# Optimization experiments

Hardware: AMD Instinct MI355X
Metric: run time of the kernel (lower is better)

Reference implementation:

```python
import jax, jax.numpy as jnp
import numpy as np

D_MODEL = 1024
NUM_HEADS = 16
D_K = D_MODEL // NUM_HEADS
D_FF = 4096
B, S = 4, 2048
EPS = 1e-5


def _linear_params(key, d_in, d_out):
    # torch nn.Linear default init: U(-1/sqrt(d_in), 1/sqrt(d_in))
    k1, k2 = jax.random.split(key)
    bound = 1.0 / np.sqrt(d_in)
    W = jax.random.uniform(k1, (d_in, d_out), jnp.float32, -bound, bound)
    b = jax.random.uniform(k2, (d_out,), jnp.float32, -bound, bound)
    return W, b


def setup_inputs() -> dict:
    key = jax.random.key(0)
    ks = jax.random.split(key, 8)
    x = jax.random.normal(ks[0], (B, S, D_MODEL), jnp.float32)
    Wq, bq = _linear_params(ks[1], D_MODEL, D_MODEL)
    Wk, bk = _linear_params(ks[2], D_MODEL, D_MODEL)
    Wv, bv = _linear_params(ks[3], D_MODEL, D_MODEL)
    Wo, bo = _linear_params(ks[4], D_MODEL, D_MODEL)
    W1, b1 = _linear_params(ks[5], D_MODEL, D_FF)
    W2, b2 = _linear_params(ks[6], D_FF, D_MODEL)
    ln1_g = jnp.ones((D_MODEL,), jnp.float32)
    ln1_b = jnp.zeros((D_MODEL,), jnp.float32)
    ln2_g = jnp.ones((D_MODEL,), jnp.float32)
    ln2_b = jnp.zeros((D_MODEL,), jnp.float32)
    return dict(x=x, Wq=Wq, bq=bq, Wk=Wk, bk=bk, Wv=Wv, bv=bv, Wo=Wo, bo=bo,
                W1=W1, b1=b1, W2=W2, b2=b2,
                ln1_g=ln1_g, ln1_b=ln1_b, ln2_g=ln2_g, ln2_b=ln2_b)


def _layernorm(x, g, b):
    mu = jnp.mean(x, axis=-1, keepdims=True)
    var = jnp.mean(jnp.square(x - mu), axis=-1, keepdims=True)
    return (x - mu) * jax.lax.rsqrt(var + EPS) * g + b


def _attention(h, Wq, bq, Wk, bk, Wv, bv, Wo, bo):
    b, s, _ = h.shape
    def split_heads(t):  # (b,s,d) -> (b,H,s,dk)
        return t.reshape(b, s, NUM_HEADS, D_K).transpose(0, 2, 1, 3)
    Q = split_heads(h @ Wq + bq)
    K = split_heads(h @ Wk + bk)
    V = split_heads(h @ Wv + bv)
    scores = jnp.einsum('bhqd,bhkd->bhqk', Q, K) / np.sqrt(D_K)
    causal = jnp.tril(jnp.ones((s, s), dtype=bool))  # True = keep
    scores = jnp.where(causal, scores, -jnp.inf)
    attn = jax.nn.softmax(scores, axis=-1)
    out = jnp.einsum('bhqk,bhkd->bhqd', attn, V)
    out = out.transpose(0, 2, 1, 3).reshape(b, s, D_MODEL)
    return out @ Wo + bo


def reference(x, Wq, bq, Wk, bk, Wv, bv, Wo, bo, W1, b1, W2, b2,
              ln1_g, ln1_b, ln2_g, ln2_b):
    # pre-norm residual block
    x = x + _attention(_layernorm(x, ln1_g, ln1_b), Wq, bq, Wk, bk, Wv, bv, Wo, bo)
    h = _layernorm(x, ln2_g, ln2_b)
    x = x + (jax.nn.relu(h @ W1 + b1) @ W2 + b2)
    return x
```

## Files before the change

kernel.cpp:

```cpp
#include <hip/hip_runtime.h>
#include <hip/hip_bf16.h>

typedef __bf16 bf16;
typedef __attribute__((ext_vector_type(8))) __bf16 bf16x8;
typedef __attribute__((ext_vector_type(4))) float f32x4;

#define D_MODEL 1024
#define NHEADS  16
#define DK      64
#define DFF     4096
#define BATCH   4
#define SEQ     2048
#define NTOK    (BATCH*SEQ)
#define QSCALE  0.18033688011112042f

__device__ __forceinline__ void gload16(const bf16* g, bf16* l) {
    __builtin_amdgcn_global_load_lds((const __attribute__((address_space(1))) void*)g,
                                     (__attribute__((address_space(3))) void*)l, 16, 0, 0);
}

__global__ __launch_bounds__(256) void transpose_cast4(
    const float* __restrict__ W0, const float* __restrict__ W1,
    const float* __restrict__ W2, const float* __restrict__ W3,
    bf16* __restrict__ T0, bf16* __restrict__ T1,
    bf16* __restrict__ T2, bf16* __restrict__ T3)
{
    const int z = blockIdx.z;
    const float* W = (z == 0) ? W0 : (z == 1) ? W1 : (z == 2) ? W2 : W3;
    bf16*       Wt = (z == 0) ? T0 : (z == 1) ? T1 : (z == 2) ? T2 : T3;
    const int K = 1024, N = 1024;
    __shared__ float tile[32][33];
    const int tx = threadIdx.x, ty = threadIdx.y;
    const int n0 = blockIdx.x * 32, k0 = blockIdx.y * 32;
#pragma unroll
    for (int i = 0; i < 4; ++i)
        tile[ty + i*8][tx] = W[(size_t)(k0 + ty + i*8) * N + n0 + tx];
    __syncthreads();
#pragma unroll
    for (int i = 0; i < 4; ++i)
        Wt[(size_t)(n0 + ty + i*8) * K + k0 + tx] = (bf16)tile[tx][ty + i*8];
}

__global__ __launch_bounds__(256) void transpose_cast(
    const float* __restrict__ W, bf16* __restrict__ Wt, int K, int N)
{
    __shared__ float tile[32][33];
    const int tx = threadIdx.x, ty = threadIdx.y;
    const int n0 = blockIdx.x * 32, k0 = blockIdx.y * 32;
#pragma unroll
    for (int i = 0; i < 4; ++i)
        tile[ty + i*8][tx] = W[(size_t)(k0 + ty + i*8) * N + n0 + tx];
    __syncthreads();
#pragma unroll
    for (int i = 0; i < 4; ++i)
        Wt[(size_t)(n0 + ty + i*8) * K + k0 + tx] = (bf16)tile[tx][ty + i*8];
}

__global__ __launch_bounds__(256) void transpose_v(
    const bf16* __restrict__ V, bf16* __restrict__ VT)
{
    __shared__ bf16 t[64][72];
    const int bh = blockIdx.y;
    const int s0 = blockIdx.x * 64;
    const int r  = threadIdx.x >> 2;
    const int c0 = (threadIdx.x & 3) * 16;
    const bf16* Vb = V  + (size_t)bh * SEQ * DK;
    bf16*       Tb = VT + (size_t)bh * DK * SEQ;
#pragma unroll
    for (int i = 0; i < 2; ++i) {
        bf16x8 v = *(const bf16x8*)&Vb[(size_t)(s0 + r) * DK + c0 + i*8];
#pragma unroll
        for (int j = 0; j < 8; ++j) t[c0 + i*8 + j][r] = v[j];
    }
    __syncthreads();
#pragma unroll
    for (int i = 0; i < 2; ++i) {
        bf16x8 o;
#pragma unroll
        for (int j = 0; j < 8; ++j) o[j] = t[r][c0 + i*8 + j];
        *(bf16x8*)&Tb[(size_t)r * SEQ + s0 + c0 + i*8] = o;
    }
}

__global__ __launch_bounds__(256) void ln_kernel(
    const float* __restrict__ x, const float* __restrict__ g,
    const float* __restrict__ beta, bf16* __restrict__ out)
{
    const int row = blockIdx.x, tid = threadIdx.x;
    const f32x4* xr = (const f32x4*)(x + (size_t)row * D_MODEL);
    f32x4 v = xr[tid];
    float s  = v[0] + v[1] + v[2] + v[3];
    float s2 = v[0]*v[0] + v[1]*v[1] + v[2]*v[2] + v[3]*v[3];
#pragma unroll
    for (int off = 32; off > 0; off >>= 1) {
        s  += __shfl_down(s,  off, 64);
        s2 += __shfl_down(s2, off, 64);
    }
    __shared__ float red[8];
    const int wave = tid >> 6, lane = tid & 63;
    if (lane == 0) { red[wave] = s; red[wave + 4] = s2; }
    __syncthreads();
    if (tid == 0) {
        float a = red[0] + red[1] + red[2] + red[3];
        float c = red[4] + red[5] + red[6] + red[7];
        float mu  = a * (1.0f / D_MODEL);
        float var = c * (1.0f / D_MODEL) - mu * mu;
        red[0] = mu;
        red[1] = rsqrtf(var + 1e-5f);
    }
    __syncthreads();
    const float mu = red[0], rs = red[1];
    f32x4 gv = ((const f32x4*)g)[tid];
    f32x4 bv = ((const f32x4*)beta)[tid];
    union { bf16 h[4]; uint2 u; } o;
#pragma unroll
    for (int i = 0; i < 4; ++i) o.h[i] = (bf16)((v[i] - mu) * rs * gv[i] + bv[i]);
    *(uint2*)(out + (size_t)row * D_MODEL + tid * 4) = o.u;
}

template<int EPI>
__global__ __launch_bounds__(256, 2) void gemm_bf16(
    const bf16* __restrict__ A, const bf16* __restrict__ Bt,
    const float* __restrict__ bias, const float* __restrict__ bias2,
    const float* __restrict__ bias3, const float* __restrict__ resid,
    void* __restrict__ outp, int M, int N, int K)
{
    __shared__ __align__(16) bf16 As[128 * 32];
    __shared__ __align__(16) bf16 Bs[128 * 32];
    const int tid  = threadIdx.x;
    const int wave = tid >> 6, lane = tid & 63;
    const int quad = lane >> 4, l16 = lane & 15;
    const int wr = wave >> 1, wc = wave & 1;
    const int m0 = blockIdx.x * 128, n0 = blockIdx.y * 128;

    const int r0 = wave * 32 + (lane >> 2);
    const int r1 = r0 + 16;
    const int u0 = ((lane & 3) - ((r0 >> 1) & 3)) & 3;
    const int u1 = ((lane & 3) - ((r1 >> 1) & 3)) & 3;
    const bf16* gA0 = A  + (size_t)(m0 + r0) * K + u0 * 8;
    const bf16* gA1 = A  + (size_t)(m0 + r1) * K + u1 * 8;
    const bf16* gB0 = Bt + (size_t)(n0 + r0) * K + u0 * 8;
    const bf16* gB1 = Bt + (size_t)(n0 + r1) * K + u1 * 8;
    bf16* lA0 = As + wave * 1024;
    bf16* lA1 = As + wave * 1024 + 512;
    bf16* lB0 = Bs + wave * 1024;
    bf16* lB1 = Bs + wave * 1024 + 512;

    int aoff[4], boff[4];
#pragma unroll
    for (int i = 0; i < 4; ++i) {
        const int ra = wr * 64 + i * 16 + l16;
        aoff[i] = ra * 32 + ((quad + ((ra >> 1) & 3)) & 3) * 8;
        const int rb = wc * 64 + i * 16 + l16;
        boff[i] = rb * 32 + ((quad + ((rb >> 1) & 3)) & 3) * 8;
    }

    const f32x4 vzero = {0.f, 0.f, 0.f, 0.f};
    f32x4 acc[4][4];
#pragma unroll
    for (int i = 0; i < 4; ++i)
#pragma unroll
        for (int j = 0; j < 4; ++j) acc[i][j] = vzero;

    for (int k0 = 0; k0 < K; k0 += 32) {
        __syncthreads();
        gload16(gA0 + k0, lA0);
        gload16(gA1 + k0, lA1);
        gload16(gB0 + k0, lB0);
        gload16(gB1 + k0, lB1);
        __syncthreads();
        bf16x8 af[4], bfr[4];
#pragma unroll
        for (int i = 0; i < 4; ++i) af[i]  = *(const bf16x8*)&As[aoff[i]];
#pragma unroll
        for (int j = 0; j < 4; ++j) bfr[j] = *(const bf16x8*)&Bs[boff[j]];
#pragma unroll
        for (int i = 0; i < 4; ++i)
#pragma unroll
            for (int j = 0; j < 4; ++j)
                acc[i][j] = __builtin_amdgcn_mfma_f32_16x16x32_bf16(af[i], bfr[j], acc[i][j], 0, 0, 0);
    }

#pragma unroll
    for (int i = 0; i < 4; ++i) {
#pragma unroll
        for (int j = 0; j < 4; ++j) {
            const int col = n0 + wc * 64 + j * 16 + l16;
            float bcol, sc = 1.0f;
            if (EPI == 0) {
                const int seg = col >> 10;
                const float* bp = (seg == 0) ? bias : ((seg == 1) ? bias2 : bias3);
                bcol = bp[col & 1023];
                if (seg == 0) sc = QSCALE;
            } else {
                bcol = bias[col];
            }
#pragma unroll
            for (int r = 0; r < 4; ++r) {
                const int row = m0 + wr * 64 + i * 16 + quad * 4 + r;
                const float v = acc[i][j][r] + bcol;
                if (EPI == 0) {
                    const int bb = row >> 11, ss = row & (SEQ - 1);
                    const int hh = (col & 1023) >> 6, dd = col & (DK - 1);
                    const size_t seg = (size_t)(col >> 10);
                    ((bf16*)outp)[seg * 8388608 + (((size_t)(bb * NHEADS + hh)) * SEQ + ss) * DK + dd] = (bf16)(v * sc);
                } else if (EPI == 1) {
                    const size_t idx = (size_t)row * N + col;
                    ((float*)outp)[idx] = v + resid[idx];
                } else {
                    ((bf16*)outp)[(size_t)row * N + col] = (bf16)fmaxf(v, 0.f);
                }
            }
        }
    }
}

#define PH_WAIT() do { \
    __builtin_amdgcn_s_barrier(); \
    asm volatile("s_waitcnt lgkmcnt(0)" ::: "memory"); \
    __builtin_amdgcn_sched_barrier(0); \
} while (0)

template<int EPI>
__global__ __launch_bounds__(512, 2) void gemm256(
    const bf16* __restrict__ A, const bf16* __restrict__ Bt,
    const float* __restrict__ bias, const float* __restrict__ bias2,
    const float* __restrict__ bias3, const float* __restrict__ resid,
    void* __restrict__ outp, int M, int N, int K)
{
    __shared__ __align__(16) bf16 smem[65536];
    const int tid  = threadIdx.x;
    const int wave = tid >> 6, lane = tid & 63;
    const int quad = lane >> 4, l16 = lane & 15;
    const int wr = wave >> 2, wcn = wave & 3;
    const int m0 = blockIdx.x * 256, n0 = blockIdx.y * 256;
    const int NT = K >> 6;

    const bf16* gA[2]; const bf16* gB[2]; int ldsOff[2];
#pragma unroll
    for (int l = 0; l < 2; ++l) {
        const int slot = tid + l * 512;
        const int r = slot >> 2;
        const int clog = (slot & 3) ^ ((r >> 1) & 3);
        gA[l] = A  + (size_t)(m0 + r) * K + clog * 8;
        gB[l] = Bt + (size_t)(n0 + r) * K + clog * 8;
        ldsOff[l] = (wave * 64 + l * 512) * 8;
    }

    auto stageA = [&](int buf, int t, int kk) {
        bf16* dst = smem + (buf * 2 + kk) * 8192;
#pragma unroll
        for (int l = 0; l < 2; ++l) gload16(gA[l] + t * 64 + kk * 32, dst + ldsOff[l]);
    };
    auto stageB = [&](int buf, int t, int kk) {
        bf16* dst = smem + 32768 + (buf * 2 + kk) * 8192;
#pragma unroll
        for (int l = 0; l < 2; ++l) gload16(gB[l] + t * 64 + kk * 32, dst + ldsOff[l]);
    };

    const int cswz  = (quad ^ ((l16 >> 1) & 3)) * 8;
    const int aBase = (wr * 128 + l16) * 32 + cswz;
    const int bBase = (wcn * 64 + l16) * 32 + cswz;

    f32x4 acc[8][4];
    const f32x4 vzero = {0.f, 0.f, 0.f, 0.f};
#pragma unroll
    for (int i = 0; i < 8; ++i)
#pragma unroll
        for (int j = 0; j < 4; ++j) acc[i][j] = vzero;

    stageA(0, 0, 0); stageB(0, 0, 0);
    stageA(0, 0, 1); stageB(0, 0, 1);
    if (NT > 1) {
        stageA(1, 1, 0); stageB(1, 1, 0);
        asm volatile("s_waitcnt vmcnt(4)" ::: "memory");
    } else {
        asm volatile("s_waitcnt vmcnt(0)" ::: "memory");
    }
    __builtin_amdgcn_s_barrier();

    bf16x8 af[4], bfr[4];
#define GMM_MFMA(mh) do { \
    __builtin_amdgcn_s_setprio(1); \
    _Pragma("unroll") \
    for (int i_ = 0; i_ < 4; ++i_) { \
        _Pragma("unroll") \
        for (int j_ = 0; j_ < 4; ++j_) \
            acc[(mh)*4 + i_][j_] = __builtin_amdgcn_mfma_f32_16x16x32_bf16(af[i_], bfr[j_], acc[(mh)*4 + i_][j_], 0, 0, 0); \
    } \
    __builtin_amdgcn_s_setprio(0); \
    __builtin_amdgcn_s_barrier(); \
} while (0)

#pragma unroll 1
    for (int t = 0; t < NT; ++t) {
        const int buf = t & 1;
        const bf16* As0 = smem + buf * 16384;
        const bf16* As1 = As0 + 8192;
        const bf16* Bs0 = smem + 32768 + buf * 16384;
        const bf16* Bs1 = Bs0 + 8192;

#pragma unroll
        for (int i = 0; i < 4; ++i) af[i]  = *(const bf16x8*)&As0[aBase + i * 512];
#pragma unroll
        for (int j = 0; j < 4; ++j) bfr[j] = *(const bf16x8*)&Bs0[bBase + j * 512];
        if (t + 1 < NT) stageA(buf ^ 1, t + 1, 1);
        PH_WAIT();
        GMM_MFMA(0);

#pragma unroll
        for (int i = 0; i < 4; ++i) af[i] = *(const bf16x8*)&As0[aBase + 2048 + i * 512];
        if (t + 1 < NT) stageB(buf ^ 1, t + 1, 1);
        PH_WAIT();
        GMM_MFMA(1);

#pragma unroll
        for (int i = 0; i < 4; ++i) af[i]  = *(const bf16x8*)&As1[aBase + 2048 + i * 512];
#pragma unroll
        for (int j = 0; j < 4; ++j) bfr[j] = *(const bf16x8*)&Bs1[bBase + j * 512];
        if (t + 2 < NT) stageA(buf, t + 2, 0);
        PH_WAIT();
        GMM_MFMA(1);

#pragma unroll
        for (int i = 0; i < 4; ++i) af[i] = *(const bf16x8*)&As1[aBase + i * 512];
        if (t + 2 < NT) {
            stageB(buf, t + 2, 0);
            asm volatile("s_waitcnt vmcnt(4)" ::: "memory");
        } else {
            asm volatile("s_waitcnt vmcnt(0)" ::: "memory");
        }
        PH_WAIT();
        GMM_MFMA(0);
    }
#undef GMM_MFMA

#pragma unroll
    for (int mf = 0; mf < 8; ++mf) {
#pragma unroll
        for (int nf = 0; nf < 4; ++nf) {
            const int col = n0 + wcn * 64 + nf * 16 + l16;
            float bcol, sc = 1.0f;
            if (EPI == 0) {
                const int seg = col >> 10;
                const float* bp = (seg == 0) ? bias : ((seg == 1) ? bias2 : bias3);
                bcol = bp[col & 1023];
                if (seg == 0) sc = QSCALE;
            } else {
                bcol = bias[col];
            }
#pragma unroll
            for (int r = 0; r < 4; ++r) {
                const int row = m0 + wr * 128 + mf * 16 + quad * 4 + r;
                const float v = acc[mf][nf][r] + bcol;
                if (EPI == 0) {
                    const int bb = row >> 11, ss = row & (SEQ - 1);
                    const int hh = (col & 1023) >> 6, dd = col & (DK - 1);
                    const size_t seg = (size_t)(col >> 10);
                    ((bf16*)outp)[seg * 8388608 + (((size_t)(bb * NHEADS + hh)) * SEQ + ss) * DK + dd] = (bf16)(v * sc);
                } else if (EPI == 1) {
                    const size_t idx = (size_t)row * N + col;
                    ((float*)outp)[idx] = v + resid[idx];
                } else {
                    ((bf16*)outp)[(size_t)row * N + col] = (bf16)fmaxf(v, 0.f);
                }
            }
        }
    }
}

__global__ __launch_bounds__(256, 2) void attn_kernel(
    const bf16* __restrict__ Q, const bf16* __restrict__ K,
    const bf16* __restrict__ VT, bf16* __restrict__ out)
{
    const int bh = blockIdx.x;
    const int b = bh >> 4, h = bh & 15;
    const int tid  = threadIdx.x;
    const int wave = tid >> 6, lane = tid & 63;
    const int quad = lane >> 4, l16 = lane & 15;

    __shared__ __align__(16) bf16 smem[32768 + 4 * 1152];
    bf16* Pw = smem + 32768 + wave * 1152;

    const bf16* Qb = Q  + (size_t)bh * SEQ * DK;
    const bf16* Kb = K  + (size_t)bh * SEQ * DK;
    const bf16* Vb = VT + (size_t)bh * DK * SEQ;

    int goK[4], goV[4], lo[4];
#pragma unroll
    for (int i = 0; i < 4; ++i) {
        const int U = (wave * 4 + i) * 64 + lane;
        const int rK = U >> 3, uK = (U & 7) ^ (rK & 7);
        goK[i] = rK * DK + uK * 8;
        const int rV = U >> 4, usw = U & 15;
        const int uV = (usw & 8) | ((usw & 7) ^ (rV & 7));
        goV[i] = rV * SEQ + uV * 8;
        lo[i]  = (wave * 4 + i) * 512;
    }

    auto stage = [&](int buf, int t) {
        const bf16* kp = Kb + (size_t)(t * 128) * DK;
        const bf16* vp = Vb + t * 128;
        bf16* kb = smem + buf * 8192;
        bf16* vb = smem + 16384 + buf * 8192;
#pragma unroll
        for (int i = 0; i < 4; ++i) gload16(kp + goK[i], kb + lo[i]);
#pragma unroll
        for (int i = 0; i < 4; ++i) gload16(vp + goV[i], vb + lo[i]);
    };

    const f32x4 vzero = {0.f, 0.f, 0.f, 0.f};
    int g = 0;
    stage(0, 0);

    for (int phase = 0; phase < 2; ++phase) {
        const int qt = phase ? (int)blockIdx.y : 15 - (int)blockIdx.y;
        const int qw = qt * 128 + wave * 32;

        bf16x8 qf[2][2];
#pragma unroll
        for (int qi = 0; qi < 2; ++qi)
#pragma unroll
            for (int kk = 0; kk < 2; ++kk)
                qf[qi][kk] = *(const bf16x8*)&Qb[(size_t)(qw + qi*16 + l16) * DK + kk*32 + quad*8];

        f32x4 Oacc[2][4];
        float m_[2], l_[2];
#pragma unroll
        for (int qi = 0; qi < 2; ++qi) {
            m_[qi] = -1.0e30f; l_[qi] = 0.f;
#pragma unroll
            for (int dj = 0; dj < 4; ++dj) Oacc[qi][dj] = vzero;
        }

        for (int t = 0; t <= qt; ++t, ++g) {
            const int cur = g & 1;
            __syncthreads();
            if (t < qt)            stage(cur ^ 1, t + 1);
            else if (phase == 0)   stage(cur ^ 1, 0);
            const bf16* kb = smem + cur * 8192;
            const bf16* vb = smem + 16384 + cur * 8192;
            const int kv0 = t * 128;

            f32x4 sv[8][2];
#pragma unroll
            for (int kvt = 0; kvt < 8; ++kvt) {
                const int R = kvt*16 + l16, rx = R & 7;
                bf16x8 kf0 = *(const bf16x8*)&kb[R*64 + (quad ^ rx)*8];
                bf16x8 kf1 = *(const bf16x8*)&kb[R*64 + (((quad + 4) & 7) ^ rx)*8];
#pragma unroll
                for (int qi = 0; qi < 2; ++qi) {
                    f32x4 tacc = vzero;
                    tacc = __builtin_amdgcn_mfma_f32_16x16x32_bf16(kf0, qf[qi][0], tacc, 0, 0, 0);
                    tacc = __builtin_amdgcn_mfma_f32_16x16x32_bf16(kf1, qf[qi][1], tacc, 0, 0, 0);
                    sv[kvt][qi] = tacc;
                }
            }

            if (t == qt) {
#pragma unroll
                for (int kvt = 0; kvt < 8; ++kvt)
#pragma unroll
                    for (int qi = 0; qi < 2; ++qi)
#pragma unroll
                        for (int r = 0; r < 4; ++r) {
                            const int kv = kv0 + kvt*16 + quad*4 + r;
                            const int q  = qw + qi*16 + l16;
                            if (kv > q) sv[kvt][qi][r] = -1.0e30f;
                        }
            }

#pragma unroll
            for (int qi = 0; qi < 2; ++qi) {
                float mx = sv[0][qi][0];
#pragma unroll
                for (int kvt = 0; kvt < 8; ++kvt)
#pragma unroll
                    for (int r = 0; r < 4; ++r) mx = fmaxf(mx, sv[kvt][qi][r]);
                mx = fmaxf(mx, __shfl_xor(mx, 16, 64));
                mx = fmaxf(mx, __shfl_xor(mx, 32, 64));
                const float newm  = fmaxf(m_[qi], mx);
                const float alpha = exp2f(m_[qi] - newm);
                m_[qi] = newm;
                float rs = 0.f;
#pragma unroll
                for (int kvt = 0; kvt < 8; ++kvt)
#pragma unroll
                    for (int r = 0; r < 4; ++r) {
                        const float p = exp2f(sv[kvt][qi][r] - newm);
                        sv[kvt][qi][r] = p;
                        rs += p;
                    }
                rs += __shfl_xor(rs, 16, 64);
                rs += __shfl_xor(rs, 32, 64);
                l_[qi] = l_[qi] * alpha + rs;
#pragma unroll
                for (int dj = 0; dj < 4; ++dj) Oacc[qi][dj] *= alpha;
            }

#pragma unroll
            for (int c2 = 0; c2 < 4; ++c2) {
#pragma unroll
                for (int qi = 0; qi < 2; ++qi)
#pragma unroll
                    for (int kl = 0; kl < 2; ++kl) {
                        union { bf16 h[4]; unsigned long long u; } pk;
                        const f32x4 s = sv[c2*2 + kl][qi];
#pragma unroll
                        for (int r = 0; r < 4; ++r) pk.h[r] = (bf16)s[r];
                        *(unsigned long long*)&Pw[(qi*16 + l16)*36 + kl*16 + quad*4] = pk.u;
                    }
                bf16x8 vf[4];
#pragma unroll
                for (int dj = 0; dj < 4; ++dj) {
                    const int R = dj*16 + l16;
                    const int u = c2*4 + quad;
                    const int usw = (u & 8) | ((u & 7) ^ (R & 7));
                    vf[dj] = *(const bf16x8*)&vb[R*128 + usw*8];
                }
#pragma unroll
                for (int qi = 0; qi < 2; ++qi) {
                    bf16x8 pf = *(const bf16x8*)&Pw[(qi*16 + l16)*36 + quad*8];
#pragma unroll
                    for (int dj = 0; dj < 4; ++dj)
                        Oacc[qi][dj] = __builtin_amdgcn_mfma_f32_16x16x32_bf16(vf[dj], pf, Oacc[qi][dj], 0, 0, 0);
                }
            }
        }

        const float inv0 = 1.0f / l_[0], inv1 = 1.0f / l_[1];
#pragma unroll
        for (int dh = 0; dh < 2; ++dh) {
#pragma unroll
            for (int qi = 0; qi < 2; ++qi) {
                const float inv = qi ? inv1 : inv0;
#pragma unroll
                for (int djl = 0; djl < 2; ++djl) {
                    const int dj = dh*2 + djl;
                    union { bf16 h[4]; unsigned long long u; } ok;
#pragma unroll
                    for (int r = 0; r < 4; ++r) ok.h[r] = (bf16)(Oacc[qi][dj][r] * inv);
                    *(unsigned long long*)&Pw[(qi*16 + l16)*36 + djl*16 + quad*4] = ok.u;
                }
            }
            const int row = lane >> 1;
#pragma unroll
            for (int it = 0; it < 2; ++it) {
                const int grp = (lane & 1) + 2*it;
                bf16x8 o = *(const bf16x8*)&Pw[row*36 + grp*8];
                *(bf16x8*)&out[((size_t)(b*SEQ + qw - wave*32 + wave*32 + row))*D_MODEL + h*DK + dh*32 + grp*8] = o;
            }
        }
    }
}

extern "C" void kernel_launch(void* const* d_in, const int* in_sizes, int n_in,
                              void* d_out, int out_size, void* d_ws, size_t ws_size,
                              hipStream_t stream)
{
    const float* x    = (const float*)d_in[0];
    const float* Wq   = (const float*)d_in[1];
    const float* bq   = (const float*)d_in[2];
    const float* Wk   = (const float*)d_in[3];
    const float* bk   = (const float*)d_in[4];
    const float* Wv   = (const float*)d_in[5];
    const float* bv   = (const float*)d_in[6];
    const float* Wo   = (const float*)d_in[7];
    const float* bo   = (const float*)d_in[8];
    const float* W1   = (const float*)d_in[9];
    const float* b1   = (const float*)d_in[10];
    const float* W2   = (const float*)d_in[11];
    const float* b2   = (const float*)d_in[12];
    const float* ln1g = (const float*)d_in[13];
    const float* ln1b = (const float*)d_in[14];
    const float* ln2g = (const float*)d_in[15];
    const float* ln2b = (const float*)d_in[16];

    char* ws = (char*)d_ws;
    const size_t MB = 1024 * 1024;
    bf16* WTq  = (bf16*)(ws + 0 * MB);
    bf16* WTk  = (bf16*)(ws + 2 * MB);
    bf16* WTv  = (bf16*)(ws + 4 * MB);
    bf16* WTo  = (bf16*)(ws + 6 * MB);
    bf16* WT1  = (bf16*)(ws + 8 * MB);
    bf16* WT2  = (bf16*)(ws + 16 * MB);
    bf16* hbuf = (bf16*)(ws + 24 * MB);
    bf16* VhT  = (bf16*)(ws + 24 * MB);
    bf16* Qh   = (bf16*)(ws + 40 * MB);
    bf16* Kh   = (bf16*)(ws + 56 * MB);
    bf16* Vh   = (bf16*)(ws + 72 * MB);
    bf16* attn = (bf16*)(ws + 88 * MB);
    bf16* ff1  = (bf16*)(ws + 40 * MB);
    float* x2  = (float*)d_out;

    dim3 tb(32, 8);
    transpose_cast4<<<dim3(32, 32, 4), tb, 0, stream>>>(Wq, Wk, Wv, Wo, WTq, WTk, WTv, WTo);
    transpose_cast<<<dim3(128, 32), tb, 0, stream>>>(W1, WT1, 1024, 4096);
    transpose_cast<<<dim3(32, 128), tb, 0, stream>>>(W2, WT2, 4096, 1024);

    ln_kernel<<<NTOK, 256, 0, stream>>>(x, ln1g, ln1b, hbuf);

    gemm256<0><<<dim3(32, 12), 512, 0, stream>>>(hbuf, WTq, bq, bk, bv, nullptr, Qh, NTOK, 3072, 1024);

    transpose_v<<<dim3(32, 64), 256, 0, stream>>>(Vh, VhT);

    attn_kernel<<<dim3(64, 8), 256, 0, stream>>>(Qh, Kh, VhT, attn);

    gemm_bf16<1><<<dim3(64, 8), 256, 0, stream>>>(attn, WTo, bo, nullptr, nullptr, x, x2, NTOK, 1024, 1024);

    ln_kernel<<<NTOK, 256, 0, stream>>>(x2, ln2g, ln2b, hbuf);

    gemm256<2><<<dim3(32, 16), 512, 0, stream>>>(hbuf, WT1, b1, nullptr, nullptr, nullptr, ff1, NTOK, 4096, 1024);
    gemm256<1><<<dim3(32, 4), 512, 0, stream>>>(ff1, WT2, b2, nullptr, nullptr, x2, x2, NTOK, 1024, 4096);
}
```

Baseline: 526.6 us.

## Add 256x128 pipelined GEMM variant for QKV, output projection and FFN2

Adds a gemm256n128 kernel: 512 threads computing a 256x128 tile, with double-buffered global-to-LDS loads split into two 32-wide K halves, s_setprio around the MFMA block, and barrier-based phase waits. It replaces the simple single-buffered 128x128 gemm_bf16 for the output projection, and replaces the 256x256 gemm256 for QKV and FFN2. The aim is more blocks per grid on the 256-CU part (256 instead of 128 for the N=1024 GEMMs) and overlap of loads with MFMA work. The cost is lower per-block reuse of the A tile than the 256x256 tile.

```diff
diff --git a/kernel.cpp b/kernel.cpp
--- a/kernel.cpp
+++ b/kernel.cpp
@@ -116,103 +116,6 @@
 #pragma unroll
     for (int i = 0; i < 4; ++i) o.h[i] = (bf16)((v[i] - mu) * rs * gv[i] + bv[i]);
     *(uint2*)(out + (size_t)row * D_MODEL + tid * 4) = o.u;
-}
-
-template<int EPI>
-__global__ __launch_bounds__(256, 2) void gemm_bf16(
-    const bf16* __restrict__ A, const bf16* __restrict__ Bt,
-    const float* __restrict__ bias, const float* __restrict__ bias2,
-    const float* __restrict__ bias3, const float* __restrict__ resid,
-    void* __restrict__ outp, int M, int N, int K)
-{
-    __shared__ __align__(16) bf16 As[128 * 32];
-    __shared__ __align__(16) bf16 Bs[128 * 32];
-    const int tid  = threadIdx.x;
-    const int wave = tid >> 6, lane = tid & 63;
-    const int quad = lane >> 4, l16 = lane & 15;
-    const int wr = wave >> 1, wc = wave & 1;
-    const int m0 = blockIdx.x * 128, n0 = blockIdx.y * 128;
-
-    const int r0 = wave * 32 + (lane >> 2);
-    const int r1 = r0 + 16;
-    const int u0 = ((lane & 3) - ((r0 >> 1) & 3)) & 3;
-    const int u1 = ((lane & 3) - ((r1 >> 1) & 3)) & 3;
-    const bf16* gA0 = A  + (size_t)(m0 + r0) * K + u0 * 8;
-    const bf16* gA1 = A  + (size_t)(m0 + r1) * K + u1 * 8;
-    const bf16* gB0 = Bt + (size_t)(n0 + r0) * K + u0 * 8;
-    const bf16* gB1 = Bt + (size_t)(n0 + r1) * K + u1 * 8;
-    bf16* lA0 = As + wave * 1024;
-    bf16* lA1 = As + wave * 1024 + 512;
-    bf16* lB0 = Bs + wave * 1024;
-    bf16* lB1 = Bs + wave * 1024 + 512;
-
-    int aoff[4], boff[4];
-#pragma unroll
-    for (int i = 0; i < 4; ++i) {
-        const int ra = wr * 64 + i * 16 + l16;
-        aoff[i] = ra * 32 + ((quad + ((ra >> 1) & 3)) & 3) * 8;
-        const int rb = wc * 64 + i * 16 + l16;
-        boff[i] = rb * 32 + ((quad + ((rb >> 1) & 3)) & 3) * 8;
-    }
-
-    const f32x4 vzero = {0.f, 0.f, 0.f, 0.f};
-    f32x4 acc[4][4];
-#pragma unroll
-    for (int i = 0; i < 4; ++i)
-#pragma unroll
-        for (int j = 0; j < 4; ++j) acc[i][j] = vzero;
-
-    for (int k0 = 0; k0 < K; k0 += 32) {
-        __syncthreads();
-        gload16(gA0 + k0, lA0);
-        gload16(gA1 + k0, lA1);
-        gload16(gB0 + k0, lB0);
-        gload16(gB1 + k0, lB1);
-        __syncthreads();
-        bf16x8 af[4], bfr[4];
-#pragma unroll
-        for (int i = 0; i < 4; ++i) af[i]  = *(const bf16x8*)&As[aoff[i]];
-#pragma unroll
-        for (int j = 0; j < 4; ++j) bfr[j] = *(const bf16x8*)&Bs[boff[j]];
-#pragma unroll
-        for (int i = 0; i < 4; ++i)
-#pragma unroll
-            for (int j = 0; j < 4; ++j)
-                acc[i][j] = __builtin_amdgcn_mfma_f32_16x16x32_bf16(af[i], bfr[j], acc[i][j], 0, 0, 0);
-    }
-
-#pragma unroll
-    for (int i = 0; i < 4; ++i) {
-#pragma unroll
-        for (int j = 0; j < 4; ++j) {
-            const int col = n0 + wc * 64 + j * 16 + l16;
-            float bcol, sc = 1.0f;
-            if (EPI == 0) {
-                const int seg = col >> 10;
-                const float* bp = (seg == 0) ? bias : ((seg == 1) ? bias2 : bias3);
-                bcol = bp[col & 1023];
-                if (seg == 0) sc = QSCALE;
-            } else {
-                bcol = bias[col];
-            }
-#pragma unroll
-            for (int r = 0; r < 4; ++r) {
-                const int row = m0 + wr * 64 + i * 16 + quad * 4 + r;
-                const float v = acc[i][j][r] + bcol;
-                if (EPI == 0) {
-                    const int bb = row >> 11, ss = row & (SEQ - 1);
-                    const int hh = (col & 1023) >> 6, dd = col & (DK - 1);
-                    const size_t seg = (size_t)(col >> 10);
-                    ((bf16*)outp)[seg * 8388608 + (((size_t)(bb * NHEADS + hh)) * SEQ + ss) * DK + dd] = (bf16)(v * sc);
-                } else if (EPI == 1) {
-                    const size_t idx = (size_t)row * N + col;
-                    ((float*)outp)[idx] = v + resid[idx];
-                } else {
-                    ((bf16*)outp)[(size_t)row * N + col] = (bf16)fmaxf(v, 0.f);
-                }
-            }
-        }
-    }
 }
 
 #define PH_WAIT() do { \
@@ -352,6 +255,146 @@
 #pragma unroll
             for (int r = 0; r < 4; ++r) {
                 const int row = m0 + wr * 128 + mf * 16 + quad * 4 + r;
+                const float v = acc[mf][nf][r] + bcol;
+                if (EPI == 0) {
+                    const int bb = row >> 11, ss = row & (SEQ - 1);
+                    const int hh = (col & 1023) >> 6, dd = col & (DK - 1);
+                    const size_t seg = (size_t)(col >> 10);
+                    ((bf16*)outp)[seg * 8388608 + (((size_t)(bb * NHEADS + hh)) * SEQ + ss) * DK + dd] = (bf16)(v * sc);
+                } else if (EPI == 1) {
+                    const size_t idx = (size_t)row * N + col;
+                    ((float*)outp)[idx] = v + resid[idx];
+                } else {
+                    ((bf16*)outp)[(size_t)row * N + col] = (bf16)fmaxf(v, 0.f);
+                }
+            }
+        }
+    }
+}
+
+template<int EPI>
+__global__ __launch_bounds__(512, 2) void gemm256n128(
+    const bf16* __restrict__ A, const bf16* __restrict__ Bt,
+    const float* __restrict__ bias, const float* __restrict__ bias2,
+    const float* __restrict__ bias3, const float* __restrict__ resid,
+    void* __restrict__ outp, int M, int N, int K)
+{
+    __shared__ __align__(16) bf16 smem[49152];
+    const int tid  = threadIdx.x;
+    const int wave = tid >> 6, lane = tid & 63;
+    const int quad = lane >> 4, l16 = lane & 15;
+    const int wr = wave >> 1, wcn = wave & 1;
+    const int m0 = blockIdx.x * 256, n0 = blockIdx.y * 128;
+    const int NT = K >> 6;
+
+    const bf16* gA[2]; const bf16* gB0; int ldsOffA[2];
+#pragma unroll
+    for (int l = 0; l < 2; ++l) {
+        const int slot = tid + l * 512;
+        const int r = slot >> 2;
+        const int clog = (slot & 3) ^ ((r >> 1) & 3);
+        gA[l] = A + (size_t)(m0 + r) * K + clog * 8;
+        ldsOffA[l] = (wave * 64 + l * 512) * 8;
+    }
+    {
+        const int r = tid >> 2;
+        const int clog = (tid & 3) ^ ((r >> 1) & 3);
+        gB0 = Bt + (size_t)(n0 + r) * K + clog * 8;
+    }
+    const int ldsOffB = wave * 512;
+
+    auto stageA = [&](int buf, int t, int kk) {
+        bf16* dst = smem + (buf * 2 + kk) * 8192;
+#pragma unroll
+        for (int l = 0; l < 2; ++l) gload16(gA[l] + t * 64 + kk * 32, dst + ldsOffA[l]);
+    };
+    auto stageB = [&](int buf, int t, int kk) {
+        bf16* dst = smem + 32768 + (buf * 2 + kk) * 4096;
+        gload16(gB0 + t * 64 + kk * 32, dst + ldsOffB);
+    };
+
+    const int cswz  = (quad ^ ((l16 >> 1) & 3)) * 8;
+    const int aBase = (wr * 64 + l16) * 32 + cswz;
+    const int bBase = (wcn * 64 + l16) * 32 + cswz;
+
+    f32x4 acc[4][4];
+    const f32x4 vzero = {0.f, 0.f, 0.f, 0.f};
+#pragma unroll
+    for (int i = 0; i < 4; ++i)
+#pragma unroll
+        for (int j = 0; j < 4; ++j) acc[i][j] = vzero;
+
+    stageA(0, 0, 0); stageB(0, 0, 0);
+    stageA(0, 0, 1); stageB(0, 0, 1);
+    if (NT > 1) {
+        stageA(1, 1, 0); stageB(1, 1, 0);
+        asm volatile("s_waitcnt vmcnt(3)" ::: "memory");
+    } else {
+        asm volatile("s_waitcnt vmcnt(0)" ::: "memory");
+    }
+    __builtin_amdgcn_s_barrier();
+
+    bf16x8 af[4], bfr[4];
+#define GMM_MFMA16() do { \
+    __builtin_amdgcn_s_setprio(1); \
+    _Pragma("unroll") \
+    for (int i_ = 0; i_ < 4; ++i_) { \
+        _Pragma("unroll") \
+        for (int j_ = 0; j_ < 4; ++j_) \
+            acc[i_][j_] = __builtin_amdgcn_mfma_f32_16x16x32_bf16(af[i_], bfr[j_], acc[i_][j_], 0, 0, 0); \
+    } \
+    __builtin_amdgcn_s_setprio(0); \
+    __builtin_amdgcn_s_barrier(); \
+} while (0)
+
+#pragma unroll 1
+    for (int t = 0; t < NT; ++t) {
+        const int buf = t & 1;
+        const bf16* As0 = smem + buf * 16384;
+        const bf16* As1 = As0 + 8192;
+        const bf16* Bs0 = smem + 32768 + buf * 8192;
+        const bf16* Bs1 = Bs0 + 4096;
+
+#pragma unroll
+        for (int i = 0; i < 4; ++i) af[i]  = *(const bf16x8*)&As0[aBase + i * 512];
+#pragma unroll
+        for (int j = 0; j < 4; ++j) bfr[j] = *(const bf16x8*)&Bs0[bBase + j * 512];
+        if (t + 1 < NT) { stageA(buf ^ 1, t + 1, 1); stageB(buf ^ 1, t + 1, 1); }
+        PH_WAIT();
+        GMM_MFMA16();
+
+#pragma unroll
+        for (int i = 0; i < 4; ++i) af[i]  = *(const bf16x8*)&As1[aBase + i * 512];
+#pragma unroll
+        for (int j = 0; j < 4; ++j) bfr[j] = *(const bf16x8*)&Bs1[bBase + j * 512];
+        if (t + 2 < NT) {
+            stageA(buf, t + 2, 0); stageB(buf, t + 2, 0);
+            asm volatile("s_waitcnt vmcnt(3)" ::: "memory");
+        } else {
+            asm volatile("s_waitcnt vmcnt(0)" ::: "memory");
+        }
+        PH_WAIT();
+        GMM_MFMA16();
+    }
+#undef GMM_MFMA16
+
+#pragma unroll
+    for (int mf = 0; mf < 4; ++mf) {
+#pragma unroll
+        for (int nf = 0; nf < 4; ++nf) {
+            const int col = n0 + wcn * 64 + nf * 16 + l16;
+            float bcol, sc = 1.0f;
+            if (EPI == 0) {
+                const int seg = col >> 10;
+                const float* bp = (seg == 0) ? bias : ((seg == 1) ? bias2 : bias3);
+                bcol = bp[col & 1023];
+                if (seg == 0) sc = QSCALE;
+            } else {
+                bcol = bias[col];
+            }
+#pragma unroll
+            for (int r = 0; r < 4; ++r) {
+                const int row = m0 + wr * 64 + mf * 16 + quad * 4 + r;
                 const float v = acc[mf][nf][r] + bcol;
                 if (EPI == 0) {
                     const int bb = row >> 11, ss = row & (SEQ - 1);
@@ -600,16 +643,16 @@
 
     ln_kernel<<<NTOK, 256, 0, stream>>>(x, ln1g, ln1b, hbuf);
 
-    gemm256<0><<<dim3(32, 12), 512, 0, stream>>>(hbuf, WTq, bq, bk, bv, nullptr, Qh, NTOK, 3072, 1024);
+    gemm256n128<0><<<dim3(32, 24), 512, 0, stream>>>(hbuf, WTq, bq, bk, bv, nullptr, Qh, NTOK, 3072, 1024);
 
     transpose_v<<<dim3(32, 64), 256, 0, stream>>>(Vh, VhT);
 
     attn_kernel<<<dim3(64, 8), 256, 0, stream>>>(Qh, Kh, VhT, attn);
 
-    gemm_bf16<1><<<dim3(64, 8), 256, 0, stream>>>(attn, WTo, bo, nullptr, nullptr, x, x2, NTOK, 1024, 1024);
+    gemm256n128<1><<<dim3(32, 8), 512, 0, stream>>>(attn, WTo, bo, nullptr, nullptr, x, x2, NTOK, 1024, 1024);
 
     ln_kernel<<<NTOK, 256, 0, stream>>>(x2, ln2g, ln2b, hbuf);
 
     gemm256<2><<<dim3(32, 16), 512, 0, stream>>>(hbuf, WT1, b1, nullptr, nullptr, nullptr, ff1, NTOK, 4096, 1024);
-    gemm256<1><<<dim3(32, 4), 512, 0, stream>>>(ff1, WT2, b2, nullptr, nullptr, x2, x2, NTOK, 1024, 4096);
-}
+    gemm256n128<1><<<dim3(32, 8), 512, 0, stream>>>(ff1, WT2, b2, nullptr, nullptr, x2, x2, NTOK, 1024, 4096);
+}
```

Result: faster. 500.0 us (-5.0%).
